# Optimization experiments

Measured on AMD Instinct MI355X. Metric: run time of the kernel, lower is better.

## Reference

```python
import jax, jax.numpy as jnp
import numpy as np

# dims
B, T1, T2, SEG = 4, 16, 16, 4          # batch, src len, tgt len, max segment length
V, E, H, ENC = 8000, 256, 256, 512     # vocab, embed, lstm hidden, encoder units
EOS = 2                                 # end-of-segment symbol ($)
NEG = -1e30                             # finite -inf (grad-safe)


def setup_inputs():
    key = jax.random.key(0)
    ks = jax.random.split(key, 16)
    s = 0.05
    n = lambda k, shp: (jax.random.normal(k, shp) * s).astype(jnp.float32)
    return {
        "prev_output_tokens": jax.random.randint(ks[0], (B, T2), 0, V),
        "encoder_outs": jax.random.normal(ks[1], (T1, B, ENC), dtype=jnp.float32),
        "embed": n(ks[2], (V, E)),
        "start_embed": n(ks[3], (E,)),
        "proj_h_w": n(ks[4], (H, ENC)), "proj_h_b": jnp.zeros((H,), jnp.float32),
        "proj_c_w": n(ks[5], (H, ENC)), "proj_c_b": jnp.zeros((H,), jnp.float32),
        "w_ih0": n(ks[6], (4 * H, H + E)), "w_hh0": n(ks[7], (4 * H, H)), "b0": jnp.zeros((4 * H,), jnp.float32),
        "w_ih1": n(ks[8], (4 * H, H)), "w_hh1": n(ks[9], (4 * H, H)), "b1": jnp.zeros((4 * H,), jnp.float32),
        "fc_w": n(ks[10], (V, H)), "fc_b": jnp.zeros((V,), jnp.float32),
    }


def _lstm_cell(x, h, c, w_ih, w_hh, b):
    # PyTorch LSTMCell gate order: i, f, g, o
    g = x @ w_ih.T + h @ w_hh.T + b
    i, f, gg, o = jnp.split(g, 4, axis=-1)
    c_new = jax.nn.sigmoid(f) * c + jax.nn.sigmoid(i) * jnp.tanh(gg)
    h_new = jax.nn.sigmoid(o) * jnp.tanh(c_new)
    return h_new, c_new


def reference(prev_output_tokens, encoder_outs, embed, start_embed,
              proj_h_w, proj_h_b, proj_c_w, proj_c_b,
              w_ih0, w_hh0, b0, w_ih1, w_hh1, b1, fc_w, fc_b):
    y = prev_output_tokens                                     # [B, T2]
    # segment windows: tok[b, t2, k] = y[b, t2+k] (clipped; masked later via logpy mask)
    pos = jnp.arange(T2 + 1)[:, None] + jnp.arange(SEG)[None, :]   # [T2+1, SEG]
    tok = y[:, jnp.minimum(pos, T2 - 1)]                            # [B, T2+1, SEG]
    emb_tok = embed[tok]                                            # [B, T2+1, SEG, E]
    x0 = jnp.broadcast_to(start_embed, (B, T2 + 1, 1, E))
    xs = jnp.moveaxis(jnp.concatenate([x0, emb_tok], axis=2), 2, 0)  # [SEG+1, B, T2+1, E]
    tgt = jnp.concatenate([tok, jnp.zeros((B, T2 + 1, 1), tok.dtype)], axis=2)
    tgt = jnp.moveaxis(tgt, 2, 0)                                    # [SEG+1, B, T2+1]

    # per-encoder-position initial states / context (encoder proj, as in __init__)
    eo = jnp.swapaxes(encoder_outs, 0, 1)                            # [B, T1, ENC]
    h0 = eo @ proj_h_w.T + proj_h_b                                  # [B, T1, H]
    c0 = eo @ proj_c_w.T + proj_c_b
    ctx = jnp.broadcast_to(h0[:, :, None, :], (B, T1, T2 + 1, H))

    def step(carry, inp):
        h1, c1, h2, c2 = carry
        x, t = inp                                                   # x [B,T2+1,E], t [B,T2+1]
        xb = jnp.broadcast_to(x[:, None, :, :], (B, T1, T2 + 1, E))
        h1, c1 = _lstm_cell(jnp.concatenate([ctx, xb], axis=-1), h1, c1, w_ih0, w_hh0, b0)
        h2, c2 = _lstm_cell(h1, h2, c2, w_ih1, w_hh1, b1)
        logp = jax.nn.log_softmax(h2 @ fc_w.T + fc_b, axis=-1)       # [B,T1,T2+1,V]
        idx = jnp.broadcast_to(t[:, None, :, None], (B, T1, T2 + 1, 1))
        sel = jnp.take_along_axis(logp, idx, axis=-1)[..., 0]
        return (h1, c1, h2, c2), (sel, logp[..., EOS])

    carry0 = (ctx,
              jnp.broadcast_to(c0[:, :, None, :], (B, T1, T2 + 1, H)),
              jnp.zeros((B, T1, T2 + 1, H), jnp.float32),
              jnp.zeros((B, T1, T2 + 1, H), jnp.float32))
    _, (sel, eosp) = jax.lax.scan(step, carry0, (xs, tgt))           # each [SEG+1,B,T1,T2+1]

    # logpy[b,t1,t2,j] = sum_{k<j} logp_k(y[t2+k]) + logp_j(EOS)
    cum = jnp.concatenate([jnp.zeros((1, B, T1, T2 + 1), sel.dtype),
                           jnp.cumsum(sel[:SEG], axis=0)], axis=0)
    logpy = jnp.moveaxis(cum + eosp, 0, -1)                          # [B,T1,T2+1,SEG+1]
    jmask = (jnp.arange(T2 + 1)[:, None] + jnp.arange(SEG + 1)[None, :]) <= T2
    logpy = jnp.where(jmask[None, None], logpy, NEG)

    # semi-Markov forward DP: alpha[t1+1, t2] = LSE_j alpha[t1, t2-j] + logpy[t1, t2-j, j]
    alpha0 = jnp.full((B, T2 + 1), NEG, sel.dtype).at[:, 0].set(0.0)

    def dp(alpha, row):                                              # row [B, T2+1, SEG+1]
        v = alpha[:, :, None] + row
        shifted = jnp.stack(
            [jnp.pad(v[:, :T2 + 1 - j, j], ((0, 0), (j, 0)), constant_values=NEG)
             for j in range(SEG + 1)], axis=0)
        return jax.nn.logsumexp(shifted, axis=0), None

    alpha, _ = jax.lax.scan(dp, alpha0, jnp.moveaxis(logpy, 1, 0))
    return alpha[:, T2]                                              # log-likelihood per batch elem
```

## Files before the change

### kernel.cpp

```cpp
#include <hip/hip_runtime.h>
#include <math.h>

#define B 4
#define T1 16
#define T2 16
#define SEG 4
#define V 8000
#define E 256
#define H 256
#define ENC 512
#define EOS 2
#define NEGV -1e30f
#define G4 1024
#define NCELL 1088
#define T21 17
#define NLT 544
#define MP 5504
#define NTM 43
#define NTN 63
#define NFCT (NTM*NTN)
#define NPART 126

typedef __attribute__((ext_vector_type(4))) float f32x4;
typedef __attribute__((ext_vector_type(8))) short bf16x8;

__device__ __forceinline__ float sigm(float x) { return 1.f / (1.f + __expf(-x)); }
__device__ __forceinline__ float ftanh(float x) { float e = __expf(2.f * x); return 1.f - 2.f / (e + 1.f); }
__device__ __forceinline__ float b2f(short x) {
    unsigned u = ((unsigned)(unsigned short)x) << 16;
    return __builtin_bit_cast(float, u);
}
__device__ __forceinline__ short f2b(float f) {
    unsigned u = __builtin_bit_cast(unsigned, f);
    unsigned r = (u + 0x7fffu + ((u >> 16) & 1u)) >> 16;
    return (short)r;
}
__device__ __forceinline__ int swz8(int row) { return (row & 7) ^ ((row & 3) << 1); }

template<int ISSUES>
__device__ __forceinline__ void stage512(const char* g0, size_t gstrideB, int kOffB, char* lds) {
    int tid = threadIdx.x;
#pragma unroll
    for (int it = 0; it < ISSUES; ++it) {
        int chunk = it * 256 + tid;
        int row = chunk >> 5;
        int g = chunk & 31;
        const char* src = g0 + (size_t)row * gstrideB + kOffB + ((g ^ swz8(row)) << 4);
        __builtin_amdgcn_global_load_lds((const __attribute__((address_space(1))) void*)src,
                                         (__attribute__((address_space(3))) void*)(lds + chunk * 16),
                                         16, 0, 0);
    }
}
template<int RSB>
__device__ __forceinline__ bf16x8 fragT(const char* lds, int row, int g) {
    return *(const bf16x8*)(lds + row * RSB + ((g ^ swz8(row)) << 4));
}

__global__ void k_setup(const float* __restrict__ fcw, const float* __restrict__ whh0,
                        const float* __restrict__ wih1, const float* __restrict__ whh1,
                        const float* __restrict__ phw, const float* __restrict__ pcw,
                        const float* __restrict__ wih0, const float* __restrict__ b1,
                        short* __restrict__ fcwbf, short* __restrict__ whh0i, short* __restrict__ w1i,
                        float* __restrict__ projhT, float* __restrict__ projcT,
                        float* __restrict__ ctxT, float* __restrict__ xT, float* __restrict__ b1i) {
    int bid = blockIdx.x, tid = threadIdx.x;
    if (bid < 2000) {
        int i = (bid * 256 + tid) * 4;
        float4 v = *(const float4*)&fcw[i];
        short4 o = { f2b(v.x), f2b(v.y), f2b(v.z), f2b(v.w) };
        *(short4*)&fcwbf[i] = o;
        return;
    }
    bid -= 2000;
    if (bid < 256) {
        int i = (bid * 256 + tid) * 4;
        int gp = i >> 8, k = i & 255;
        float4 v = *(const float4*)&whh0[(size_t)((gp & 3) * 256 + (gp >> 2)) * 256 + k];
        short4 o = { f2b(v.x), f2b(v.y), f2b(v.z), f2b(v.w) };
        *(short4*)&whh0i[i] = o;
        return;
    }
    bid -= 256;
    if (bid < 512) {
        int i = (bid * 256 + tid) * 4;
        int gp = i >> 9, k = i & 511;
        int g = (gp & 3) * 256 + (gp >> 2);
        const float* src = (k < 256) ? &wih1[(size_t)g * 256 + k] : &whh1[(size_t)g * 256 + (k - 256)];
        float4 v = *(const float4*)src;
        short4 o = { f2b(v.x), f2b(v.y), f2b(v.z), f2b(v.w) };
        *(short4*)&w1i[i] = o;
        return;
    }
    bid -= 512;
    if (bid < 128) {
        int i = (bid * 256 + tid) * 4;
        int k = i >> 8, r = i & 255;
        float4 o = { phw[(size_t)r * ENC + k], phw[(size_t)(r + 1) * ENC + k],
                     phw[(size_t)(r + 2) * ENC + k], phw[(size_t)(r + 3) * ENC + k] };
        *(float4*)&projhT[i] = o;
        return;
    }
    bid -= 128;
    if (bid < 128) {
        int i = (bid * 256 + tid) * 4;
        int k = i >> 8, r = i & 255;
        float4 o = { pcw[(size_t)r * ENC + k], pcw[(size_t)(r + 1) * ENC + k],
                     pcw[(size_t)(r + 2) * ENC + k], pcw[(size_t)(r + 3) * ENC + k] };
        *(float4*)&projcT[i] = o;
        return;
    }
    bid -= 128;
    if (bid < 512) {
        int i = (bid * 256 + tid) * 4;
        int g = i >> 9, k = i & 511;
        float4 v = *(const float4*)&wih0[i];
        float* base = (k < 256) ? &ctxT[(size_t)k * G4 + g] : &xT[(size_t)(k - 256) * G4 + g];
        base[0] = v.x; base[G4] = v.y; base[2 * G4] = v.z; base[3 * G4] = v.w;
        return;
    }
    bid -= 512;
    if (bid < 1) {
        float4 o = { b1[tid], b1[256 + tid], b1[512 + tid], b1[768 + tid] };
        *(float4*)&b1i[tid * 4] = o;
    }
}

__global__ void k_init1(const int* __restrict__ y, const float* __restrict__ embed, const float* __restrict__ se,
                        const float* __restrict__ enc, const float* __restrict__ phT,
                        const float* __restrict__ phb, const float* __restrict__ pcT,
                        const float* __restrict__ pcb, const float* __restrict__ xT,
                        float* __restrict__ h0p, float* __restrict__ c0p, float* __restrict__ pre_xi) {
    __shared__ float sb[256];
    int bid = blockIdx.x, j = threadIdx.x;
    if (bid < 256) {
        int q = bid & 3, bi = bid >> 2;
        int b = bi / T1, i = bi % T1;
        if (j < 128) sb[j] = enc[(size_t)(i * B + b) * ENC + q * 128 + j];
        __syncthreads();
        float ha = (q == 0) ? phb[j] : 0.f;
        float ca = (q == 0) ? pcb[j] : 0.f;
        for (int e = 0; e < 128; ++e) {
            float x = sb[e];
            ha += x * phT[(size_t)(q * 128 + e) * H + j];
            ca += x * pcT[(size_t)(q * 128 + e) * H + j];
        }
        h0p[(size_t)(q * 64 + bi) * H + j] = ha;
        c0p[(size_t)(q * 64 + bi) * H + j] = ca;
        return;
    }
    int row = bid - 256;
    int s = row / (B * T21), rem = row % (B * T21);
    int b = rem / T21, t = rem % T21;
    const float* src;
    if (s == 0) src = se;
    else { int tt = t + s - 1; if (tt > 15) tt = 15; src = embed + (size_t)y[b * T2 + tt] * E; }
    sb[j] = src[j];
    __syncthreads();
    float a0 = 0, a1 = 0, a2 = 0, a3 = 0;
    for (int k = 0; k < E; ++k) {
        float x = sb[k];
        const float* w = xT + (size_t)k * G4;
        a0 += x * w[j]; a1 += x * w[256 + j]; a2 += x * w[512 + j]; a3 += x * w[768 + j];
    }
    *(float4*)&pre_xi[(size_t)row * G4 + 4 * j] = make_float4(a0, a1, a2, a3);
}

__global__ void k_init2(const float* __restrict__ h0p, const float* __restrict__ c0p,
                        const float* __restrict__ ctxT, const float* __restrict__ b0,
                        float* __restrict__ c1, float* __restrict__ c2,
                        short* __restrict__ hcA, short* __restrict__ hcB,
                        float* __restrict__ pre_ctxi) {
    __shared__ float sb[256];
    int bid = blockIdx.x, j = threadIdx.x;
    if (bid < NCELL) {
        int cell = bid, bi = cell / T21;
        float hv = 0.f, cv = 0.f;
#pragma unroll
        for (int q = 0; q < 4; ++q) {
            hv += h0p[(size_t)(q * 64 + bi) * H + j];
            cv += c0p[(size_t)(q * 64 + bi) * H + j];
        }
        c1[(size_t)cell * H + j] = cv;
        c2[(size_t)cell * H + j] = 0.f;
        hcA[(size_t)cell * 512 + j] = f2b(hv);
        hcB[(size_t)cell * 512 + 256 + j] = 0;
        return;
    }
    int bi = bid - NCELL;
    float hv = 0.f;
#pragma unroll
    for (int q = 0; q < 4; ++q) hv += h0p[(size_t)(q * 64 + bi) * H + j];
    sb[j] = hv;
    __syncthreads();
    float a0 = b0[j], a1 = b0[256 + j], a2 = b0[512 + j], a3 = b0[768 + j];
    for (int k = 0; k < H; ++k) {
        float x = sb[k];
        const float* w = ctxT + (size_t)k * G4;
        a0 += x * w[j]; a1 += x * w[256 + j]; a2 += x * w[512 + j]; a3 += x * w[768 + j];
    }
    *(float4*)&pre_ctxi[(size_t)bi * G4 + 4 * j] = make_float4(a0, a1, a2, a3);
}

__device__ __forceinline__ void mma32(const char* smA, const char* smB,
                                      int wm, int wn2, int ln, int kg, f32x4 acc[2]) {
#pragma unroll
    for (int ks = 0; ks < 8; ++ks) {
        bf16x8 a = fragT<512>(smA, wm * 16 + ln, ks * 4 + kg);
#pragma unroll
        for (int nf = 0; nf < 2; ++nf) {
            bf16x8 b = fragT<512>(smB, wn2 * 32 + nf * 16 + ln, ks * 4 + kg);
            acc[nf] = __builtin_amdgcn_mfma_f32_16x16x32_bf16(a, b, acc[nf], 0, 0, 0);
        }
    }
}

__device__ __forceinline__ void lstm0_body(int step, int l, char* smA, char* smB,
        const short* __restrict__ IN, const short* __restrict__ whh0i,
        const float* __restrict__ pre_ctxi, const float* __restrict__ pre_xi,
        float* __restrict__ c1, short* __restrict__ OUT) {
    int tid = threadIdx.x;
    int wave = tid >> 6, lane = tid & 63, ln = lane & 15, kg = lane >> 4;
    int wm = wave & 1, wn2 = wave >> 1;
    int mb = l >> 4, nb = l & 15;
    int m0 = mb * 32, n0 = nb * 64;
    stage512<4>((const char*)(IN + (size_t)m0 * 512), 1024, 0, smA);
    stage512<8>((const char*)(whh0i + (size_t)n0 * 256), 512, 0, smB);
    __syncthreads();
    f32x4 acc[2] = {};
    mma32(smA, smB, wm, wn2, ln, kg, acc);
    __syncthreads();
    float* sg = (float*)smA;
#pragma unroll
    for (int nf = 0; nf < 2; ++nf)
#pragma unroll
        for (int r = 0; r < 4; ++r)
            sg[(wm * 16 + kg * 4 + r) * 68 + wn2 * 32 + nf * 16 + ln] = acc[nf][r];
    __syncthreads();
    int jlo = nb * 16;
#pragma unroll
    for (int q2 = 0; q2 < 2; ++q2) {
        int item = q2 * 256 + tid;
        int c = item >> 4, jj = item & 15;
        int cell = m0 + c;
        int j = jlo + jj;
        float4 g = *(float4*)&sg[c * 68 + 4 * jj];
        int bi = cell / T21;
        int bb = bi >> 4;
        int t = cell % T21;
        int prow = (step * B + bb) * T21 + t;
        float4 pc = *(const float4*)&pre_ctxi[(size_t)bi * G4 + 4 * j];
        float4 px = *(const float4*)&pre_xi[(size_t)prow * G4 + 4 * j];
        float ig = g.x + pc.x + px.x, fg = g.y + pc.y + px.y;
        float gg = g.z + pc.z + px.z, og = g.w + pc.w + px.w;
        float cold = c1[(size_t)cell * H + j];
        float cn = sigm(fg) * cold + sigm(ig) * ftanh(gg);
        float hn = sigm(og) * ftanh(cn);
        c1[(size_t)cell * H + j] = cn;
        OUT[(size_t)cell * 512 + j] = f2b(hn);
    }
}

__device__ __forceinline__ void lstm1_body(int l, char* smA, char* smB,
        const short* __restrict__ IN, const short* __restrict__ w1i,
        const float* __restrict__ b1i, float* __restrict__ c2,
        short* __restrict__ slab, short* __restrict__ OUT, bool writeOUT) {
    int tid = threadIdx.x;
    int wave = tid >> 6, lane = tid & 63, ln = lane & 15, kg = lane >> 4;
    int wm = wave & 1, wn2 = wave >> 1;
    int mb = l >> 4, nb = l & 15;
    int m0 = mb * 32, n0 = nb * 64;
    f32x4 acc[2] = {};
#pragma unroll
    for (int kh = 0; kh < 2; ++kh) {
        if (kh) __syncthreads();
        stage512<4>((const char*)(IN + (size_t)m0 * 512), 1024, kh * 512, smA);
        stage512<8>((const char*)(w1i + (size_t)n0 * 512), 1024, kh * 512, smB);
        __syncthreads();
        mma32(smA, smB, wm, wn2, ln, kg, acc);
    }
    __syncthreads();
    float* sg = (float*)smA;
#pragma unroll
    for (int nf = 0; nf < 2; ++nf)
#pragma unroll
        for (int r = 0; r < 4; ++r)
            sg[(wm * 16 + kg * 4 + r) * 68 + wn2 * 32 + nf * 16 + ln] = acc[nf][r];
    __syncthreads();
    int jlo = nb * 16;
#pragma unroll
    for (int q2 = 0; q2 < 2; ++q2) {
        int item = q2 * 256 + tid;
        int c = item >> 4, jj = item & 15;
        int cell = m0 + c;
        int j = jlo + jj;
        float4 g = *(float4*)&sg[c * 68 + 4 * jj];
        float4 bv = *(const float4*)&b1i[4 * j];
        float ig = g.x + bv.x, fg = g.y + bv.y, gg = g.z + bv.z, og = g.w + bv.w;
        float cold = c2[(size_t)cell * H + j];
        float cn = sigm(fg) * cold + sigm(ig) * ftanh(gg);
        float hn = sigm(og) * ftanh(cn);
        c2[(size_t)cell * H + j] = cn;
        short hb = f2b(hn);
        slab[(size_t)cell * 256 + j] = hb;
        if (writeOUT) OUT[(size_t)cell * 512 + 256 + j] = hb;
    }
}

__global__ __launch_bounds__(256, 3) void k_lstm(int s, int n_l1, int wout,
        const short* __restrict__ IN, short* __restrict__ OUT, short* __restrict__ slab,
        const short* __restrict__ whh0i, const short* __restrict__ w1i,
        const float* __restrict__ pre_ctxi, const float* __restrict__ pre_xi,
        const float* __restrict__ b1i, float* __restrict__ c1, float* __restrict__ c2) {
    __shared__ __align__(16) char smem[49152];
    char* smA = smem;
    char* smB = smem + 16384;
    int bx = blockIdx.x;
    if (bx < n_l1) lstm1_body(bx, smA, smB, IN, w1i, b1i, c2, slab, OUT, wout != 0);
    else lstm0_body(s + 1, bx - n_l1, smA, smB, IN, whh0i, pre_ctxi, pre_xi, c1, OUT);
}

__global__ __launch_bounds__(256, 4) void k_fc(const short* __restrict__ h2base, const short* __restrict__ Wv,
        const float* __restrict__ fcb, float* __restrict__ psum) {
    __shared__ __align__(16) char smem[32768];
    char* smA = smem;
    char* smB = smem + 16384;
    int bx = blockIdx.x;
    int xcd = bx & 7, idx = bx >> 3;
    int q = NFCT >> 3, r = NFCT & 7;
    int tl = xcd * q + (xcd < r ? xcd : r) + idx;
    int nb = tl / NTM, mb = tl % NTM;
    int m0 = mb * 128, n0 = nb * 128;
    int tid = threadIdx.x;
    int wave = tid >> 6, lane = tid & 63, ln = lane & 15, kg = lane >> 4;
    int wm = wave >> 1, wn = wave & 1;
    f32x4 acc[4][4] = {};
#pragma unroll
    for (int kq = 0; kq < 4; ++kq) {
        if (kq) __syncthreads();
#pragma unroll
        for (int it = 0; it < 4; ++it) {
            int chunk = it * 256 + tid;
            int row = chunk >> 3;
            int g = chunk & 7;
            const char* src = (const char*)(h2base + (size_t)(m0 + row) * 256)
                              + kq * 128 + ((g ^ swz8(row)) << 4);
            __builtin_amdgcn_global_load_lds((const __attribute__((address_space(1))) void*)src,
                                             (__attribute__((address_space(3))) void*)(smA + chunk * 16),
                                             16, 0, 0);
        }
#pragma unroll
        for (int it = 0; it < 4; ++it) {
            int chunk = it * 256 + tid;
            int row = chunk >> 3;
            int g = chunk & 7;
            int grow = n0 + row; if (grow > V - 1) grow = V - 1;
            const char* src = (const char*)(Wv + (size_t)grow * 256)
                              + kq * 128 + ((g ^ swz8(row)) << 4);
            __builtin_amdgcn_global_load_lds((const __attribute__((address_space(1))) void*)src,
                                             (__attribute__((address_space(3))) void*)(smB + chunk * 16),
                                             16, 0, 0);
        }
        __syncthreads();
#pragma unroll
        for (int ks = 0; ks < 2; ++ks) {
            bf16x8 a[4], b[4];
#pragma unroll
            for (int mf = 0; mf < 4; ++mf) a[mf] = fragT<128>(smA, wm * 64 + mf * 16 + ln, ks * 4 + kg);
#pragma unroll
            for (int nf = 0; nf < 4; ++nf) b[nf] = fragT<128>(smB, wn * 64 + nf * 16 + ln, ks * 4 + kg);
#pragma unroll
            for (int mf = 0; mf < 4; ++mf)
#pragma unroll
                for (int nf = 0; nf < 4; ++nf)
                    acc[mf][nf] = __builtin_amdgcn_mfma_f32_16x16x32_bf16(a[mf], b[nf], acc[mf][nf], 0, 0, 0);
        }
    }
    float rs[4][4];
#pragma unroll
    for (int mf = 0; mf < 4; ++mf)
#pragma unroll
        for (int r2 = 0; r2 < 4; ++r2) rs[mf][r2] = 0.f;
#pragma unroll
    for (int nf = 0; nf < 4; ++nf) {
        int col = n0 + wn * 64 + nf * 16 + ln;
        float fbn = (col < V) ? fcb[col] : NEGV;
#pragma unroll
        for (int mf = 0; mf < 4; ++mf)
#pragma unroll
            for (int r2 = 0; r2 < 4; ++r2)
                rs[mf][r2] += __expf(acc[mf][nf][r2] + fbn);
    }
#pragma unroll
    for (int mask = 1; mask < 16; mask <<= 1)
#pragma unroll
        for (int mf = 0; mf < 4; ++mf)
#pragma unroll
            for (int r2 = 0; r2 < 4; ++r2)
                rs[mf][r2] += __shfl_xor(rs[mf][r2], mask);
    if (ln == 0) {
#pragma unroll
        for (int mf = 0; mf < 4; ++mf)
#pragma unroll
            for (int r2 = 0; r2 < 4; ++r2)
                psum[(size_t)(nb * 2 + wn) * MP + m0 + wm * 64 + mf * 16 + kg * 4 + r2] = rs[mf][r2];
    }
}

__global__ void k_combine(const short* __restrict__ h2all, const short* __restrict__ Wv,
        const float* __restrict__ fcb, const int* __restrict__ y,
        const float* __restrict__ psum, float* __restrict__ sel, float* __restrict__ eosp) {
    int cb = blockIdx.x;
    int s = cb / 17, blk = cb % 17;
    int tid = threadIdx.x;
    int cl = tid >> 2, q = tid & 3;
    int cell = blk * 64 + cl;
    int b = cell / (T1 * T21);
    int t = cell % T21;
    int tv = 0;
    if (s < SEG) { int tt = t + s; if (tt > 15) tt = 15; tv = y[b * T2 + tt]; }
    const short* hp = h2all + (size_t)(s + 1) * NCELL * 256 + (size_t)cell * 256 + q * 64;
    const short* w1 = Wv + (size_t)tv * 256 + q * 64;
    const short* w2 = Wv + (size_t)EOS * 256 + q * 64;
    float d1 = 0.f, d2 = 0.f;
#pragma unroll
    for (int u = 0; u < 8; ++u) {
        bf16x8 av  = *(const bf16x8*)(hp + u * 8);
        bf16x8 wv1 = *(const bf16x8*)(w1 + u * 8);
        bf16x8 wv2 = *(const bf16x8*)(w2 + u * 8);
#pragma unroll
        for (int e = 0; e < 8; ++e) {
            float a = b2f(av[e]);
            d1 += a * b2f(wv1[e]);
            d2 += a * b2f(wv2[e]);
        }
    }
    d1 += __shfl_xor(d1, 1); d1 += __shfl_xor(d1, 2);
    d2 += __shfl_xor(d2, 1); d2 += __shfl_xor(d2, 2);
    int col = s * NCELL + cell;
    float ss = 0.f;
    for (int v2 = q * 32; v2 < q * 32 + 32 && v2 < NPART; ++v2)
        ss += psum[(size_t)v2 * MP + col];
    ss += __shfl_xor(ss, 1); ss += __shfl_xor(ss, 2);
    if (q == 0) {
        float lse = __logf(ss);
        sel[s * NCELL + cell]  = d1 + fcb[tv]  - lse;
        eosp[s * NCELL + cell] = d2 + fcb[EOS] - lse;
    }
}

__global__ void k_dp(const float* __restrict__ sel, const float* __restrict__ eosp, float* __restrict__ out) {
    __shared__ float row[SEG + 1][NCELL];
    __shared__ float alpha[B][T21];
    int tid = threadIdx.x;
    for (int c = tid; c < NCELL; c += 256) {
        float cum = 0.f;
        row[0][c] = eosp[c];
#pragma unroll
        for (int j = 1; j <= SEG; ++j) {
            cum += sel[(j - 1) * NCELL + c];
            row[j][c] = cum + eosp[j * NCELL + c];
        }
    }
    int b = tid / T21, t = tid % T21;
    bool act = tid < B * T21;
    if (act) alpha[b][t] = (t == 0) ? 0.f : NEGV;
    __syncthreads();
    for (int i = 0; i < T1; ++i) {
        float val = NEGV;
        if (act) {
            float terms[SEG + 1];
            float mx = -3.4e38f;
            int cnt2 = 0;
            for (int j = 0; j <= SEG && j <= t; ++j) {
                int cell = (b * T1 + i) * T21 + (t - j);
                float term = alpha[b][t - j] + row[j][cell];
                terms[cnt2++] = term;
                mx = fmaxf(mx, term);
            }
            float ssum = 0.f;
            for (int k2 = 0; k2 < cnt2; ++k2) ssum += __expf(terms[k2] - mx);
            val = mx + __logf(ssum);
        }
        __syncthreads();
        if (act) alpha[b][t] = val;
        __syncthreads();
    }
    if (act && t == T2) out[b] = alpha[b][T2];
}

extern "C" void kernel_launch(void* const* d_in, const int* in_sizes, int n_in,
                              void* d_out, int out_size, void* d_ws, size_t ws_size,
                              hipStream_t stream) {
    const int*   y     = (const int*)d_in[0];
    const float* enc   = (const float*)d_in[1];
    const float* embed = (const float*)d_in[2];
    const float* se    = (const float*)d_in[3];
    const float* phw   = (const float*)d_in[4];
    const float* phb   = (const float*)d_in[5];
    const float* pcw   = (const float*)d_in[6];
    const float* pcb   = (const float*)d_in[7];
    const float* wih0  = (const float*)d_in[8];
    const float* whh0  = (const float*)d_in[9];
    const float* b0    = (const float*)d_in[10];
    const float* wih1  = (const float*)d_in[11];
    const float* whh1  = (const float*)d_in[12];
    const float* b1    = (const float*)d_in[13];
    const float* fcw   = (const float*)d_in[14];
    const float* fcb   = (const float*)d_in[15];

    float* ws = (float*)d_ws;
    size_t off = 0;
    auto alloc = [&](size_t n) { float* p = ws + off; off += n; return p; };
    float* projhT   = alloc((size_t)ENC * H);
    float* projcT   = alloc((size_t)ENC * H);
    float* ctxT     = alloc((size_t)H * G4);
    float* xT       = alloc((size_t)E * G4);
    float* h0p      = alloc((size_t)4 * 64 * H);
    float* c0p      = alloc((size_t)4 * 64 * H);
    float* pre_ctxi = alloc((size_t)B * T1 * G4);
    float* pre_xi   = alloc((size_t)(SEG + 1) * B * T21 * G4);
    float* c1       = alloc((size_t)NCELL * H);
    float* c2       = alloc((size_t)NCELL * H);
    float* b1i      = alloc((size_t)G4);
    float* selbuf   = alloc((size_t)(SEG + 1) * NCELL);
    float* eospbuf  = alloc((size_t)(SEG + 1) * NCELL);
    float* psum     = alloc((size_t)NPART * MP);
    short* hc0      = (short*)alloc((size_t)NCELL * 512 / 2);
    short* hc1      = (short*)alloc((size_t)NCELL * 512 / 2);
    short* h2all    = (short*)alloc(((size_t)6 * NCELL + 64) * 256 / 2);
    short* whh0i    = (short*)alloc((size_t)G4 * 256 / 2);
    short* w1i      = (short*)alloc((size_t)G4 * 512 / 2);
    short* fcwbf    = (short*)alloc((size_t)V * H / 2);

    hipLaunchKernelGGL(k_setup, dim3(3537), dim3(256), 0, stream,
                       fcw, whh0, wih1, whh1, phw, pcw, wih0, b1,
                       fcwbf, whh0i, w1i, projhT, projcT, ctxT, xT, b1i);
    hipLaunchKernelGGL(k_init1, dim3(256 + (SEG + 1) * B * T21), dim3(256), 0, stream,
                       y, embed, se, enc, projhT, phb, projcT, pcb, xT, h0p, c0p, pre_xi);
    hipLaunchKernelGGL(k_init2, dim3(NCELL + 64), dim3(256), 0, stream,
                       h0p, c0p, ctxT, b0, c1, c2, hc0, hc1, pre_ctxi);

    short* hcb[2] = { hc0, hc1 };
    hipLaunchKernelGGL(k_lstm, dim3(NLT), dim3(256), 0, stream,
                       -1, 0, 1, hcb[0], hcb[1], h2all,
                       whh0i, w1i, pre_ctxi, pre_xi, b1i, c1, c2);
    for (int s = 0; s < SEG; ++s) {
        hipLaunchKernelGGL(k_lstm, dim3(2 * NLT), dim3(256), 0, stream,
                           s, NLT, 1, hcb[(s + 1) & 1], hcb[s & 1],
                           h2all + (size_t)(s + 1) * NCELL * 256,
                           whh0i, w1i, pre_ctxi, pre_xi, b1i, c1, c2);
    }
    hipLaunchKernelGGL(k_lstm, dim3(NLT), dim3(256), 0, stream,
                       4, NLT, 0, hcb[1], hcb[0],
                       h2all + (size_t)5 * NCELL * 256,
                       whh0i, w1i, pre_ctxi, pre_xi, b1i, c1, c2);

    hipLaunchKernelGGL(k_fc, dim3(NFCT), dim3(256), 0, stream,
                       h2all + (size_t)NCELL * 256, fcwbf, fcb, psum);
    hipLaunchKernelGGL(k_combine, dim3(85), dim3(256), 0, stream,
                       h2all, fcwbf, fcb, y, psum, selbuf, eospbuf);
    hipLaunchKernelGGL(k_dp, dim3(1), dim3(256), 0, stream, selbuf, eospbuf, (float*)d_out);
}
```

Before: 173.6 us.

## Fuse FC tiles and combine into LSTM step launches to overlap stages

Merges the LSTM, FC GEMM, combine and fcw bf16 cast into one multi-role kernel launched once per step. FC row-blocks and combine blocks for slabs that are already finished run in the same grid as later LSTM steps. The fcw cast moves out of setup into the first step. The goal is to fill idle CUs during the small LSTM launches and to drop separate launches, at the cost of a larger register and LDS footprint and a more fragile per-launch scheduling of block ranges.

```diff
diff --git a/kernel.cpp b/kernel.cpp
--- a/kernel.cpp
+++ b/kernel.cpp
@@ -18,8 +18,8 @@
 #define MP 5504
 #define NTM 43
 #define NTN 63
-#define NFCT (NTM*NTN)
 #define NPART 126
+#define SLAB ((size_t)NCELL * 256)
 
 typedef __attribute__((ext_vector_type(4))) float f32x4;
 typedef __attribute__((ext_vector_type(8))) short bf16x8;
@@ -56,22 +56,14 @@
     return *(const bf16x8*)(lds + row * RSB + ((g ^ swz8(row)) << 4));
 }
 
-__global__ void k_setup(const float* __restrict__ fcw, const float* __restrict__ whh0,
+__global__ void k_setup(const float* __restrict__ whh0,
                         const float* __restrict__ wih1, const float* __restrict__ whh1,
                         const float* __restrict__ phw, const float* __restrict__ pcw,
                         const float* __restrict__ wih0, const float* __restrict__ b1,
-                        short* __restrict__ fcwbf, short* __restrict__ whh0i, short* __restrict__ w1i,
+                        short* __restrict__ whh0i, short* __restrict__ w1i,
                         float* __restrict__ projhT, float* __restrict__ projcT,
                         float* __restrict__ ctxT, float* __restrict__ xT, float* __restrict__ b1i) {
     int bid = blockIdx.x, tid = threadIdx.x;
-    if (bid < 2000) {
-        int i = (bid * 256 + tid) * 4;
-        float4 v = *(const float4*)&fcw[i];
-        short4 o = { f2b(v.x), f2b(v.y), f2b(v.z), f2b(v.w) };
-        *(short4*)&fcwbf[i] = o;
-        return;
-    }
-    bid -= 2000;
     if (bid < 256) {
         int i = (bid * 256 + tid) * 4;
         int gp = i >> 8, k = i & 255;
@@ -306,29 +298,15 @@
     }
 }
 
-__global__ __launch_bounds__(256, 3) void k_lstm(int s, int n_l1, int wout,
-        const short* __restrict__ IN, short* __restrict__ OUT, short* __restrict__ slab,
-        const short* __restrict__ whh0i, const short* __restrict__ w1i,
-        const float* __restrict__ pre_ctxi, const float* __restrict__ pre_xi,
-        const float* __restrict__ b1i, float* __restrict__ c1, float* __restrict__ c2) {
-    __shared__ __align__(16) char smem[49152];
+__device__ __forceinline__ void fc_body(int bx, int mbLo, int nmb, int nfc, char* smem,
+        const short* __restrict__ h2base, const short* __restrict__ Wv,
+        const float* __restrict__ fcb, float* __restrict__ psum) {
     char* smA = smem;
     char* smB = smem + 16384;
-    int bx = blockIdx.x;
-    if (bx < n_l1) lstm1_body(bx, smA, smB, IN, w1i, b1i, c2, slab, OUT, wout != 0);
-    else lstm0_body(s + 1, bx - n_l1, smA, smB, IN, whh0i, pre_ctxi, pre_xi, c1, OUT);
-}
-
-__global__ __launch_bounds__(256, 4) void k_fc(const short* __restrict__ h2base, const short* __restrict__ Wv,
-        const float* __restrict__ fcb, float* __restrict__ psum) {
-    __shared__ __align__(16) char smem[32768];
-    char* smA = smem;
-    char* smB = smem + 16384;
-    int bx = blockIdx.x;
     int xcd = bx & 7, idx = bx >> 3;
-    int q = NFCT >> 3, r = NFCT & 7;
+    int q = nfc >> 3, r = nfc & 7;
     int tl = xcd * q + (xcd < r ? xcd : r) + idx;
-    int nb = tl / NTM, mb = tl % NTM;
+    int nb = tl / nmb, mb = mbLo + tl % nmb;
     int m0 = mb * 128, n0 = nb * 128;
     int tid = threadIdx.x;
     int wave = tid >> 6, lane = tid & 63, ln = lane & 15, kg = lane >> 4;
@@ -406,10 +384,10 @@
     }
 }
 
-__global__ void k_combine(const short* __restrict__ h2all, const short* __restrict__ Wv,
+__device__ __forceinline__ void combine_body(int cb,
+        const short* __restrict__ h2all, const short* __restrict__ Wv,
         const float* __restrict__ fcb, const int* __restrict__ y,
         const float* __restrict__ psum, float* __restrict__ sel, float* __restrict__ eosp) {
-    int cb = blockIdx.x;
     int s = cb / 17, blk = cb % 17;
     int tid = threadIdx.x;
     int cl = tid >> 2, q = tid & 3;
@@ -418,7 +396,7 @@
     int t = cell % T21;
     int tv = 0;
     if (s < SEG) { int tt = t + s; if (tt > 15) tt = 15; tv = y[b * T2 + tt]; }
-    const short* hp = h2all + (size_t)(s + 1) * NCELL * 256 + (size_t)cell * 256 + q * 64;
+    const short* hp = h2all + (size_t)(s + 1) * SLAB + (size_t)cell * 256 + q * 64;
     const short* w1 = Wv + (size_t)tv * 256 + q * 64;
     const short* w2 = Wv + (size_t)EOS * 256 + q * 64;
     float d1 = 0.f, d2 = 0.f;
@@ -445,6 +423,40 @@
         float lse = __logf(ss);
         sel[s * NCELL + cell]  = d1 + fcb[tv]  - lse;
         eosp[s * NCELL + cell] = d2 + fcb[EOS] - lse;
+    }
+}
+
+struct SA {
+    const short* whh0i; const short* w1i;
+    const float* pre_ctxi; const float* pre_xi; const float* b1i;
+    float* c1; float* c2;
+    short* h2all;
+    const short* fcwbf; const float* fcb; const int* y;
+    float* psum; float* sel; float* eosp;
+    const float* fcw; short* fcwbf_out;
+};
+
+__global__ __launch_bounds__(256, 3) void k_step(SA a,
+        int nl1, int s1, int wout, int nl0, int s0,
+        const short* IN, short* OUT, short* slab,
+        int mbLo, int nmb, int nfc, int cmbLo, int ncmb, int ncast) {
+    __shared__ __align__(16) char smem[49152];
+    char* smA = smem;
+    char* smB = smem + 16384;
+    int bx = blockIdx.x;
+    if (bx < nl1) { lstm1_body(bx, smA, smB, IN, a.w1i, a.b1i, a.c2, slab, OUT, wout != 0); return; }
+    bx -= nl1;
+    if (bx < nl0) { lstm0_body(s0, bx, smA, smB, IN, a.whh0i, a.pre_ctxi, a.pre_xi, a.c1, OUT); return; }
+    bx -= nl0;
+    if (bx < nfc) { fc_body(bx, mbLo, nmb, nfc, smem, a.h2all + SLAB, a.fcwbf, a.fcb, a.psum); return; }
+    bx -= nfc;
+    if (bx < ncmb) { combine_body(cmbLo + bx, a.h2all, a.fcwbf, a.fcb, a.y, a.psum, a.sel, a.eosp); return; }
+    bx -= ncmb;
+    if (bx < ncast) {
+        int i = (bx * 256 + threadIdx.x) * 4;
+        float4 v = *(const float4*)&a.fcw[i];
+        short4 o = { f2b(v.x), f2b(v.y), f2b(v.z), f2b(v.w) };
+        *(short4*)&a.fcwbf_out[i] = o;
     }
 }
 
@@ -532,32 +544,35 @@
     short* w1i      = (short*)alloc((size_t)G4 * 512 / 2);
     short* fcwbf    = (short*)alloc((size_t)V * H / 2);
 
-    hipLaunchKernelGGL(k_setup, dim3(3537), dim3(256), 0, stream,
-                       fcw, whh0, wih1, whh1, phw, pcw, wih0, b1,
-                       fcwbf, whh0i, w1i, projhT, projcT, ctxT, xT, b1i);
+    hipLaunchKernelGGL(k_setup, dim3(1537), dim3(256), 0, stream,
+                       whh0, wih1, whh1, phw, pcw, wih0, b1,
+                       whh0i, w1i, projhT, projcT, ctxT, xT, b1i);
     hipLaunchKernelGGL(k_init1, dim3(256 + (SEG + 1) * B * T21), dim3(256), 0, stream,
                        y, embed, se, enc, projhT, phb, projcT, pcb, xT, h0p, c0p, pre_xi);
     hipLaunchKernelGGL(k_init2, dim3(NCELL + 64), dim3(256), 0, stream,
                        h0p, c0p, ctxT, b0, c1, c2, hc0, hc1, pre_ctxi);
 
-    short* hcb[2] = { hc0, hc1 };
-    hipLaunchKernelGGL(k_lstm, dim3(NLT), dim3(256), 0, stream,
-                       -1, 0, 1, hcb[0], hcb[1], h2all,
-                       whh0i, w1i, pre_ctxi, pre_xi, b1i, c1, c2);
-    for (int s = 0; s < SEG; ++s) {
-        hipLaunchKernelGGL(k_lstm, dim3(2 * NLT), dim3(256), 0, stream,
-                           s, NLT, 1, hcb[(s + 1) & 1], hcb[s & 1],
-                           h2all + (size_t)(s + 1) * NCELL * 256,
-                           whh0i, w1i, pre_ctxi, pre_xi, b1i, c1, c2);
-    }
-    hipLaunchKernelGGL(k_lstm, dim3(NLT), dim3(256), 0, stream,
-                       4, NLT, 0, hcb[1], hcb[0],
-                       h2all + (size_t)5 * NCELL * 256,
-                       whh0i, w1i, pre_ctxi, pre_xi, b1i, c1, c2);
-
-    hipLaunchKernelGGL(k_fc, dim3(NFCT), dim3(256), 0, stream,
-                       h2all + (size_t)NCELL * 256, fcwbf, fcb, psum);
-    hipLaunchKernelGGL(k_combine, dim3(85), dim3(256), 0, stream,
-                       h2all, fcwbf, fcb, y, psum, selbuf, eospbuf);
+    SA a;
+    a.whh0i = whh0i; a.w1i = w1i; a.pre_ctxi = pre_ctxi; a.pre_xi = pre_xi; a.b1i = b1i;
+    a.c1 = c1; a.c2 = c2; a.h2all = h2all; a.fcwbf = fcwbf; a.fcb = fcb; a.y = y;
+    a.psum = psum; a.sel = selbuf; a.eosp = eospbuf; a.fcw = fcw; a.fcwbf_out = fcwbf;
+
+    hipLaunchKernelGGL(k_step, dim3(NLT + 2000), dim3(256), 0, stream, a,
+                       0, -1, 0, NLT, 0, hc0, hc1, h2all, 0, 1, 0, 0, 0, 2000);
+    hipLaunchKernelGGL(k_step, dim3(2 * NLT), dim3(256), 0, stream, a,
+                       NLT, 0, 1, NLT, 1, hc1, hc0, h2all + SLAB, 0, 1, 0, 0, 0, 0);
+    hipLaunchKernelGGL(k_step, dim3(2 * NLT + 504), dim3(256), 0, stream, a,
+                       NLT, 1, 1, NLT, 2, hc0, hc1, h2all + 2 * SLAB, 0, 8, 504, 0, 0, 0);
+    hipLaunchKernelGGL(k_step, dim3(2 * NLT + 567), dim3(256), 0, stream, a,
+                       NLT, 2, 1, NLT, 3, hc1, hc0, h2all + 3 * SLAB, 8, 9, 567, 0, 0, 0);
+    hipLaunchKernelGGL(k_step, dim3(2 * NLT + 504 + 34), dim3(256), 0, stream, a,
+                       NLT, 3, 1, NLT, 4, hc0, hc1, h2all + 4 * SLAB, 17, 8, 504, 0, 34, 0);
+    hipLaunchKernelGGL(k_step, dim3(NLT + 567), dim3(256), 0, stream, a,
+                       NLT, 4, 0, 0, -1, hc1, hc0, h2all + 5 * SLAB, 25, 9, 567, 0, 0, 0);
+    hipLaunchKernelGGL(k_step, dim3(567 + 34), dim3(256), 0, stream, a,
+                       0, -1, 0, 0, -1, hc1, hc0, h2all, 34, 9, 567, 34, 34, 0);
+    hipLaunchKernelGGL(k_step, dim3(17), dim3(256), 0, stream, a,
+                       0, -1, 0, 0, -1, hc1, hc0, h2all, 0, 1, 0, 68, 17, 0);
+
     hipLaunchKernelGGL(k_dp, dim3(1), dim3(256), 0, stream, selbuf, eospbuf, (float*)d_out);
 }
```

Result: slower. 181.3 us (+4.4%).
